# Optimization experiments

Hardware: AMD Instinct MI355X
Metric: run time of the kernel (lower is better)

The kernel has to match this reference:

```python
import jax, jax.numpy as jnp
import numpy as np

DT = 0.1
B_SZ = 8192
T_HIST = 20
LEN_PRED = 30
FEAT = 32
N_LAYERS = 3
# state transition for constant-acceleration model (matches self.F in torch)
F_MAT = np.array([[1.0, DT, DT * DT / 2], [0.0, 1.0, DT], [0.0, 0.0, 1.0]], dtype=np.float32)


def setup_inputs() -> dict:
    key = jax.random.key(0)
    ks = jax.random.split(key, 16)
    # random-walk trajectories as history observations
    hist = jnp.cumsum(jax.random.normal(ks[0], (B_SZ, T_HIST, 2), jnp.float32) * 0.5, axis=1)
    k_lin = 1.0 / np.sqrt(FEAT)
    k_in = 1.0 / np.sqrt(24)

    def u(k, shape, scale):
        return jax.random.uniform(k, shape, jnp.float32, -scale, scale)

    return {
        "hist": hist,
        "max_accel_x": jnp.ones((1,), jnp.float32) * 10.0,
        "max_accel_y": jnp.ones((1,), jnp.float32) * 20.0,
        "velocity_std_x": jnp.ones((1,), jnp.float32) * 10.0,
        "acceleration_std_x": jnp.ones((1,), jnp.float32) * 10.0,
        "R_x_": jnp.array([0.0448], jnp.float32),
        "R_y_": jnp.array([0.001], jnp.float32),
        "G_x": jnp.array([0.0059, 0.2981, 0.0393], jnp.float32),
        "G_y": jnp.array([0.0059, 0.2981, 0.0393], jnp.float32) / 5.0,
        "Win_W": u(ks[1], (FEAT, 24), k_in),
        "Win_b": u(ks[2], (FEAT,), k_in),
        "enc_Wih": u(ks[3], (N_LAYERS, 4 * FEAT, FEAT), k_lin),
        "enc_Whh": u(ks[4], (N_LAYERS, 4 * FEAT, FEAT), k_lin),
        "enc_bih": u(ks[5], (N_LAYERS, 4 * FEAT), k_lin),
        "enc_bhh": u(ks[6], (N_LAYERS, 4 * FEAT), k_lin),
        "dec_Wih": u(ks[7], (N_LAYERS, 4 * FEAT, FEAT), k_lin),
        "dec_Whh": u(ks[8], (N_LAYERS, 4 * FEAT, FEAT), k_lin),
        "dec_bih": u(ks[9], (N_LAYERS, 4 * FEAT), k_lin),
        "dec_bhh": u(ks[10], (N_LAYERS, 4 * FEAT), k_lin),
        "Wout_W": u(ks[11], (4, FEAT), k_lin),
        "Wout_b": u(ks[12], (4,), k_lin),
        "len_pred": LEN_PRED,
    }


def reference(hist, max_accel_x, max_accel_y, velocity_std_x, acceleration_std_x,
              R_x_, R_y_, G_x, G_y, Win_W, Win_b,
              enc_Wih, enc_Whh, enc_bih, enc_bhh,
              dec_Wih, dec_Whh, dec_bih, dec_bhh,
              Wout_W, Wout_b, len_pred):
    B = hist.shape[0]
    F = jnp.asarray(F_MAT)
    R_x = R_x_[0] * R_x_[0]
    R_y = R_y_[0] * R_y_[0]
    Z_x = hist[:, :, 0]
    Z_y = hist[:, :, 1]

    def lstm(x, h, c, Wih, Whh, bih, bhh):
        g = x @ Wih.T + bih + h @ Whh.T + bhh
        i, f, gg, o = jnp.split(g, 4, axis=1)
        c = jax.nn.sigmoid(f) * c + jax.nn.sigmoid(i) * jnp.tanh(gg)
        h = jax.nn.sigmoid(o) * jnp.tanh(c)
        return h, c

    def stack(XP, h, c, Wih, Whh, bih, bhh):
        x = jnp.tanh(XP @ Win_W.T + Win_b)
        hs, cs = [], []
        for j in range(N_LAYERS):
            hj, cj = lstm(x, h[j], c[j], Wih[j], Whh[j], bih[j], bhh[j])
            hs.append(hj)
            cs.append(cj)
            x = cj  # torch code feeds the fresh CELL state to the next layer
        return jnp.stack(hs), jnp.stack(cs)

    def kpred(X, P, Q):
        return X @ F.T, jnp.einsum('ij,bjk,lk->bil', F, P, F) + Q

    def kupdate(X, P, z, R):
        y = z - X[:, 0]                      # innovation (H picks component 0)
        S = P[:, 0, 0] + R                   # innovation covariance (scalar)
        K = P[:, :, 0] / S[:, None]          # Kalman gain (B,3)
        return X + y[:, None] * K, P - K[:, :, None] * P[:, 0:1, :]

    def kinit(z0):
        # torch always calls _kalman_init with is_x=True (default), so both
        # axes use R_x / velocity_std_x / acceleration_std_x
        X = jnp.zeros((B, 3), hist.dtype).at[:, 0].set(z0)
        d = jnp.stack([R_x, velocity_std_x[0] ** 2, acceleration_std_x[0] ** 2])
        P = jnp.zeros((B, 3, 3), hist.dtype).at[:, jnp.arange(3), jnp.arange(3)].set(d)
        return X, P

    Qx_e = jnp.outer(G_x * max_accel_x[0], G_x * max_accel_x[0])
    Qy_e = jnp.outer(G_y * max_accel_y[0], G_y * max_accel_y[0])

    Xx, Px = kinit(Z_x[:, 0])
    Xy, Py = kinit(Z_y[:, 0])
    h = jnp.zeros((N_LAYERS, B, FEAT), hist.dtype)
    c = jnp.zeros_like(h)

    def enc_step(carry, zs):
        Xx, Px, Xy, Py, h, c = carry
        zx, zy = zs
        XP = jnp.concatenate([Xx, Xy, Px.reshape(B, 9), Py.reshape(B, 9)], 1)
        h, c = stack(XP, h, c, enc_Wih, enc_Whh, enc_bih, enc_bhh)
        Xx, Px = kpred(Xx, Px, Qx_e)
        Xy, Py = kpred(Xy, Py, Qy_e)
        Xx, Px = kupdate(Xx, Px, zx, R_x)
        Xy, Py = kupdate(Xy, Py, zy, R_y)
        return (Xx, Px, Xy, Py, h, c), None

    carry, _ = jax.lax.scan(enc_step, (Xx, Px, Xy, Py, h, c),
                            (Z_x[:, 1:].T, Z_y[:, 1:].T))

    oxx = jnp.outer(G_x, G_x)
    oyy = jnp.outer(G_y, G_y)

    def dec_step(carry, _):
        Xx, Px, Xy, Py, h, c = carry
        XP = jnp.concatenate([Xx, Xy, Px.reshape(B, 9), Py.reshape(B, 9)], 1)
        h, c = stack(XP, h, c, dec_Wih, dec_Whh, dec_bih, dec_bhh)
        pred = c[-1] @ Wout_W.T + Wout_b  # (B,4): [u_x, u_y, std_x, std_y]
        Xx = Xx.at[:, 2].set(DT * pred[:, 0])  # X[:,2] = B*u
        Xy = Xy.at[:, 2].set(DT * pred[:, 1])
        Qx = (pred[:, 2] ** 2)[:, None, None] * oxx
        Qy = (pred[:, 3] ** 2)[:, None, None] * oyy
        Xx, Px = kpred(Xx, Px, Qx)
        Xy, Py = kpred(Xy, Py, Qy)
        out = jnp.stack([Xx[:, 0], Xy[:, 0],
                         jnp.sqrt(Px[:, 0, 0]), jnp.sqrt(Py[:, 0, 0]),
                         jnp.zeros(B, hist.dtype)], axis=1)  # (B,5)
        return (Xx, Px, Xy, Py, h, c), out

    carry, ys = jax.lax.scan(dec_step, carry, None, length=len_pred)
    return jnp.transpose(ys, (1, 0, 2))  # (B, len_pred, 5)
```

## Files before the change

### kernel.cpp

```cpp
#include <hip/hip_runtime.h>
#include <math.h>

#define DT   0.1f
#define HDT  0.005f
#define T_HIST 20
#define LEN_PRED 30
#define NLOG2E   (-1.4426950408889634f)
#define TWOLOG2E ( 2.8853900817779268f)

typedef __attribute__((ext_vector_type(8))) short bfrag8;
typedef __attribute__((ext_vector_type(4))) float f32x4;

#define WS_FRAG  0u
#define WS_WIN   98304u
#define WS_WOUT  100352u
#define WS_BIASC 101376u
#define WS_WINC  102912u
#define WS_WOUTB 103040u

static __device__ __forceinline__ unsigned short f2bf(float x) {
    union { float f; unsigned int u; } v; v.f = x;
    unsigned int r = v.u + 0x7fffu + ((v.u >> 16) & 1u);
    return (unsigned short)(r >> 16);
}

static __device__ __forceinline__ unsigned int pack2bf(float lo, float hi) {
    unsigned int ul = __float_as_uint(lo) + 0x8000u;
    unsigned int uh = __float_as_uint(hi) + 0x8000u;
    return __builtin_amdgcn_perm(uh, ul, 0x07060302u);
}

static __device__ __forceinline__ float rcp1(float z) {
    return __builtin_amdgcn_rcpf(1.f + __builtin_amdgcn_exp2f(z));
}
static __device__ __forceinline__ float th_(float z) {
    return fmaf(-2.f, rcp1(z), 1.f);
}

__global__ void prep_kernel(const float* __restrict__ Win_W, const float* __restrict__ Win_b,
                            const float* __restrict__ eWih, const float* __restrict__ eWhh,
                            const float* __restrict__ ebih, const float* __restrict__ ebhh,
                            const float* __restrict__ dWih, const float* __restrict__ dWhh,
                            const float* __restrict__ dbih, const float* __restrict__ dbhh,
                            const float* __restrict__ Wout_W, const float* __restrict__ Wout_b,
                            char* __restrict__ ws)
{
    int i = blockIdx.x * blockDim.x + threadIdx.x;
    if (i < 49152) {
        int fi = i >> 9, w = i & 511;
        int lane = w >> 3, jj = w & 7;
        int c = fi & 1, j = (fi >> 1) & 7, pl = fi >> 4;
        int l = pl % 3, ph = pl / 3;
        int mm = lane & 15, qq = lane >> 4;
        int gate = mm & 3;
        int row = gate * 32 + 8 * (mm >> 2) + j;
        int k = qq * 8 + jj;
        float scale = (gate == 2) ? TWOLOG2E : NLOG2E;
        const float* W = c ? (ph ? dWhh : eWhh) : (ph ? dWih : eWih);
        ((unsigned short*)(ws + WS_FRAG))[i] = f2bf(W[l * 4096 + row * 32 + k] * scale);
    } else if (i < 50176) {
        int i2 = i - 49152;
        int T = i2 >> 9, w = i2 & 511;
        int lane = w >> 3, jj = w & 7;
        int mm = lane & 15, qq = lane >> 4;
        int feat = 8 * (mm >> 2) + 4 * T + (mm & 3);
        int k = qq * 8 + jj;
        float v = (k < 24) ? Win_W[feat * 24 + k] * TWOLOG2E : 0.f;
        ((unsigned short*)(ws + WS_WIN))[i2] = f2bf(v);
    } else if (i < 50688) {
        int i3 = i - 50176;
        int lane = i3 >> 3, jj = i3 & 7;
        int mm = lane & 15, qq = lane >> 4;
        float v = (mm < 4) ? Wout_W[mm * 32 + qq * 8 + jj] : 0.f;
        ((unsigned short*)(ws + WS_WOUT))[i3] = f2bf(v);
    } else if (i < 51072) {
        int b = i - 50688;
        int r = b & 3, qq = (b >> 2) & 3, j = (b >> 4) & 7, pl = b >> 7;
        int l = pl % 3, ph = pl / 3;
        int row = r * 32 + 8 * qq + j;
        float scale = (r == 2) ? TWOLOG2E : NLOG2E;
        const float* bi = ph ? dbih : ebih;
        const float* bh = ph ? dbhh : ebhh;
        ((float*)(ws + WS_BIASC))[b] = (bi[l * 128 + row] + bh[l * 128 + row]) * scale;
    } else if (i < 51104) {
        int b = i - 51072;
        int r = b & 3, qq = (b >> 2) & 3, T = b >> 4;
        ((float*)(ws + WS_WINC))[b] = Win_b[8 * qq + 4 * T + r] * TWOLOG2E;
    } else if (i < 51108) {
        ((float*)(ws + WS_WOUTB))[i - 51104] = Wout_b[i - 51104];
    }
}

__launch_bounds__(64)
__global__ void kalman_lstm_kernel(const float* __restrict__ hist,
                                   const float* __restrict__ max_ax, const float* __restrict__ max_ay,
                                   const float* __restrict__ vstd, const float* __restrict__ astd,
                                   const float* __restrict__ Rx_, const float* __restrict__ Ry_,
                                   const float* __restrict__ Gx, const float* __restrict__ Gy,
                                   const char* __restrict__ ws, float* __restrict__ out)
{
    __shared__ unsigned short xp[16][40];

    const int lane = threadIdx.x;
    const int q = lane >> 4, m = lane & 15, ch = q & 1;
    const int b_elem = blockIdx.x * 16 + m;

    for (int i = lane; i < 640; i += 64) (&xp[0][0])[i] = 0;
    __builtin_amdgcn_wave_barrier();

    bfrag8 fragA[3][8][2];
    f32x4  biasC[3][8];
    const bfrag8* fragp = (const bfrag8*)(ws + WS_FRAG);
    const f32x4*  biasp = (const f32x4*)(ws + WS_BIASC);
    auto load_phase = [&](int ph) {
#pragma unroll
        for (int l = 0; l < 3; ++l)
#pragma unroll
            for (int j = 0; j < 8; ++j) {
#pragma unroll
                for (int c = 0; c < 2; ++c)
                    fragA[l][j][c] = fragp[(((ph * 3 + l) * 8 + j) * 2 + c) * 64 + lane];
                biasC[l][j] = biasp[((ph * 3 + l) * 8 + j) * 4 + q];
            }
    };
    load_phase(0);

    bfrag8 winF0 = ((const bfrag8*)(ws + WS_WIN))[lane];
    bfrag8 winF1 = ((const bfrag8*)(ws + WS_WIN))[64 + lane];
    f32x4  winC0 = ((const f32x4*)(ws + WS_WINC))[q];
    f32x4  winC1 = ((const f32x4*)(ws + WS_WINC))[4 + q];
    bfrag8 woutF = ((const bfrag8*)(ws + WS_WOUT))[lane];
    const float* wbp = (const float*)(ws + WS_WOUTB);
    const float wb0 = wbp[0], wb1 = wbp[1], wb2 = wbp[2], wb3 = wbp[3];

    const float rx = Rx_[0] * Rx_[0], ry = Ry_[0] * Ry_[0];
    const float Rch = ch ? ry : rx;
    float g0, g1, g2, s;
    if (ch == 0) { g0 = Gx[0]; g1 = Gx[1]; g2 = Gx[2]; s = max_ax[0]; }
    else         { g0 = Gy[0]; g1 = Gy[1]; g2 = Gy[2]; s = max_ay[0]; }
    const float ge0 = g0 * s, ge1 = g1 * s, ge2 = g2 * s;
    float X0 = (q < 2) ? hist[b_elem * 40 + ch] : 0.f;
    float X1 = 0.f, X2 = 0.f;
    float P00 = Rch, P01 = 0.f, P02 = 0.f;
    float P11 = vstd[0] * vstd[0], P12 = 0.f, P22 = astd[0] * astd[0];

    union { unsigned int u[4]; bfrag8 v; } zf; zf.u[0] = zf.u[1] = zf.u[2] = zf.u[3] = 0;
    bfrag8 hfrag[3] = { zf.v, zf.v, zf.v };
    float cst[3][8];
#pragma unroll
    for (int l = 0; l < 3; ++l)
#pragma unroll
        for (int j = 0; j < 8; ++j) cst[l][j] = 0.f;
    bfrag8 xfrag = zf.v;

    auto kpred = [&](float Q00, float Q01, float Q02, float Q11, float Q12, float Q22) {
        X0 = X0 + DT * X1 + HDT * X2;
        X1 = X1 + DT * X2;
        float M00 = P00 + DT * P01 + HDT * P02;
        float M01 = P01 + DT * P11 + HDT * P12;
        float M02 = P02 + DT * P12 + HDT * P22;
        float M11 = P11 + DT * P12;
        float M12 = P12 + DT * P22;
        float M22 = P22;
        P00 = M00 + DT * M01 + HDT * M02 + Q00;
        P01 = M01 + DT * M02 + Q01;
        P02 = M02 + Q02;
        P11 = M11 + DT * M12 + Q11;
        P12 = M12 + Q12;
        P22 = M22 + Q22;
    };
    auto kupdate = [&](float z) {
        float y = z - X0;
        float Sinv = 1.0f / (P00 + Rch);
        float K0 = P00 * Sinv, K1 = P01 * Sinv, K2 = P02 * Sinv;
        X0 += y * K0; X1 += y * K1; X2 += y * K2;
        float p00 = P00, p01 = P01, p02 = P02;
        P00 = p00 - K0 * p00;
        P01 = p01 - K0 * p01;
        P02 = p02 - K0 * p02;
        P11 = P11 - K1 * p01;
        P12 = P12 - K1 * p02;
        P22 = P22 - K2 * p02;
    };

    auto stack = [&]() {
        if (q < 2) {
            unsigned short* row = &xp[m][0];
            int o = ch * 3;
            row[o + 0] = f2bf(X0); row[o + 1] = f2bf(X1); row[o + 2] = f2bf(X2);
            int pb = 6 + ch * 9;
            row[pb + 0] = f2bf(P00); row[pb + 1] = f2bf(P01); row[pb + 2] = f2bf(P02);
            row[pb + 3] = f2bf(P01); row[pb + 4] = f2bf(P11); row[pb + 5] = f2bf(P12);
            row[pb + 6] = f2bf(P02); row[pb + 7] = f2bf(P12); row[pb + 8] = f2bf(P22);
        }
        __builtin_amdgcn_wave_barrier();
        bfrag8 bxp = *(const bfrag8*)&xp[m][q * 8];
        __builtin_amdgcn_wave_barrier();
        f32x4 t0 = __builtin_amdgcn_mfma_f32_16x16x32_bf16(winF0, bxp, winC0, 0, 0, 0);
        f32x4 t1 = __builtin_amdgcn_mfma_f32_16x16x32_bf16(winF1, bxp, winC1, 0, 0, 0);
        union { unsigned int u[4]; bfrag8 v; } xu;
        xu.u[0] = pack2bf(th_(t0[0]), th_(t0[1]));
        xu.u[1] = pack2bf(th_(t0[2]), th_(t0[3]));
        xu.u[2] = pack2bf(th_(t1[0]), th_(t1[1]));
        xu.u[3] = pack2bf(th_(t1[2]), th_(t1[3]));
        xfrag = xu.v;
#pragma unroll
        for (int l = 0; l < 3; ++l) {
            f32x4 acc[8];
#pragma unroll
            for (int j = 0; j < 8; ++j) {
                f32x4 hh = __builtin_amdgcn_mfma_f32_16x16x32_bf16(fragA[l][j][1], hfrag[l], biasC[l][j], 0, 0, 0);
                acc[j]   = __builtin_amdgcn_mfma_f32_16x16x32_bf16(fragA[l][j][0], xfrag, hh, 0, 0, 0);
            }
            union { unsigned int u[4]; bfrag8 v; } xu2, hu2;
#pragma unroll
            for (int jp = 0; jp < 4; ++jp) {
                float cn[2], hn[2];
#pragma unroll
                for (int e = 0; e < 2; ++e) {
                    int j = jp * 2 + e;
                    float iv = rcp1(acc[j][0]);
                    float fv = rcp1(acc[j][1]);
                    float gv = th_(acc[j][2]);
                    float ov = rcp1(acc[j][3]);
                    float cv = fmaf(fv, cst[l][j], iv * gv);
                    cst[l][j] = cv;
                    float tc = th_(cv * TWOLOG2E);
                    cn[e] = cv; hn[e] = ov * tc;
                }
                xu2.u[jp] = pack2bf(cn[0], cn[1]);
                hu2.u[jp] = pack2bf(hn[0], hn[1]);
            }
            xfrag = xu2.v;
            hfrag[l] = hu2.v;
        }
    };

    const f32x4 zero4 = {0.f, 0.f, 0.f, 0.f};

    float znext = (q < 2) ? hist[b_elem * 40 + 2 + ch] : 0.f;
#pragma unroll 1
    for (int t = 0; t < T_HIST - 1; ++t) {
        stack();
        float z = znext;
        if (t < 18) znext = (q < 2) ? hist[b_elem * 40 + (t + 2) * 2 + ch] : 0.f;
        kpred(ge0 * ge0, ge0 * ge1, ge0 * ge2, ge1 * ge1, ge1 * ge2, ge2 * ge2);
        kupdate(z);
    }

    load_phase(1);

#pragma unroll 1
    for (int t = 0; t < LEN_PRED; ++t) {
        stack();
        f32x4 ap = __builtin_amdgcn_mfma_f32_16x16x32_bf16(woutF, xfrag, zero4, 0, 0, 0);
        float s0 = __shfl(ap[0] + wb0, m);
        float s1 = __shfl(ap[1] + wb1, m);
        float s2 = __shfl(ap[2] + wb2, m);
        float s3 = __shfl(ap[3] + wb3, m);
        float pe = ch ? s1 : s0;
        float qe = ch ? s3 : s2;
        X2 = DT * pe;
        float qs = qe * qe;
        kpred(qs * g0 * g0, qs * g0 * g1, qs * g0 * g2, qs * g1 * g1, qs * g1 * g2, qs * g2 * g2);
        if (q < 2) {
            float* o = out + (size_t)b_elem * (LEN_PRED * 5) + t * 5;
            if (ch == 0) { o[0] = X0; o[2] = sqrtf(P00); }
            else         { o[1] = X0; o[3] = sqrtf(P00); o[4] = 0.f; }
        }
    }
}

extern "C" void kernel_launch(void* const* d_in, const int* in_sizes, int n_in,
                              void* d_out, int out_size, void* d_ws, size_t ws_size,
                              hipStream_t stream)
{
    const float* hist  = (const float*)d_in[0];
    const float* maxax = (const float*)d_in[1];
    const float* maxay = (const float*)d_in[2];
    const float* vstd  = (const float*)d_in[3];
    const float* astd  = (const float*)d_in[4];
    const float* Rx    = (const float*)d_in[5];
    const float* Ry    = (const float*)d_in[6];
    const float* Gx    = (const float*)d_in[7];
    const float* Gy    = (const float*)d_in[8];
    const float* WinW  = (const float*)d_in[9];
    const float* Winb  = (const float*)d_in[10];
    const float* eWih  = (const float*)d_in[11];
    const float* eWhh  = (const float*)d_in[12];
    const float* ebih  = (const float*)d_in[13];
    const float* ebhh  = (const float*)d_in[14];
    const float* dWih  = (const float*)d_in[15];
    const float* dWhh  = (const float*)d_in[16];
    const float* dbih  = (const float*)d_in[17];
    const float* dbhh  = (const float*)d_in[18];
    const float* WoutW = (const float*)d_in[19];
    const float* Woutb = (const float*)d_in[20];
    char* ws = (char*)d_ws;
    float* out = (float*)d_out;

    prep_kernel<<<200, 256, 0, stream>>>(WinW, Winb, eWih, eWhh, ebih, ebhh,
                                         dWih, dWhh, dbih, dbhh, WoutW, Woutb, ws);
    kalman_lstm_kernel<<<512, 64, 0, stream>>>(hist, maxax, maxay, vstd, astd,
                                               Rx, Ry, Gx, Gy, ws, out);
}
```

Baseline: 217.1 us.

## Halve batch per wave and split LSTM cell nonlinearities across half-lanes

Each wave now handles 8 batch elements instead of 16, and the grid doubles to 1024 waves. Lanes with m>=8 take over the elementwise gate math for feature columns 4-7 via shfl_xor, halving the serial transcendental work per lane. Results are exchanged back with shuffles to rebuild the bf16 fragments. The trade is twice the MFMA work overall (half the MFMA columns are wasted) and extra shuffles, in exchange for shorter per-step latency and more waves to fill the GPU.

```diff
diff --git a/kernel.cpp b/kernel.cpp
--- a/kernel.cpp
+++ b/kernel.cpp
@@ -103,7 +103,8 @@
 
     const int lane = threadIdx.x;
     const int q = lane >> 4, m = lane & 15, ch = q & 1;
-    const int b_elem = blockIdx.x * 16 + m;
+    const bool act = (m < 8);
+    const int b_elem = blockIdx.x * 8 + (m & 7);
 
     for (int i = lane; i < 640; i += 64) (&xp[0][0])[i] = 0;
     __builtin_amdgcn_wave_barrier();
@@ -139,19 +140,19 @@
     if (ch == 0) { g0 = Gx[0]; g1 = Gx[1]; g2 = Gx[2]; s = max_ax[0]; }
     else         { g0 = Gy[0]; g1 = Gy[1]; g2 = Gy[2]; s = max_ay[0]; }
     const float ge0 = g0 * s, ge1 = g1 * s, ge2 = g2 * s;
-    float X0 = (q < 2) ? hist[b_elem * 40 + ch] : 0.f;
+    float X0 = (q < 2 && act) ? hist[b_elem * 40 + ch] : 0.f;
     float X1 = 0.f, X2 = 0.f;
     float P00 = Rch, P01 = 0.f, P02 = 0.f;
     float P11 = vstd[0] * vstd[0], P12 = 0.f, P22 = astd[0] * astd[0];
 
     union { unsigned int u[4]; bfrag8 v; } zf; zf.u[0] = zf.u[1] = zf.u[2] = zf.u[3] = 0;
     bfrag8 hfrag[3] = { zf.v, zf.v, zf.v };
-    float cst[3][8];
+    bfrag8 xfrag = zf.v;
+    float cst[3][4];
 #pragma unroll
     for (int l = 0; l < 3; ++l)
 #pragma unroll
-        for (int j = 0; j < 8; ++j) cst[l][j] = 0.f;
-    bfrag8 xfrag = zf.v;
+        for (int k = 0; k < 4; ++k) cst[l][k] = 0.f;
 
     auto kpred = [&](float Q00, float Q01, float Q02, float Q11, float Q12, float Q22) {
         X0 = X0 + DT * X1 + HDT * X2;
@@ -184,7 +185,7 @@
     };
 
     auto stack = [&]() {
-        if (q < 2) {
+        if (q < 2 && act) {
             unsigned short* row = &xp[m][0];
             int o = ch * 3;
             row[o + 0] = f2bf(X0); row[o + 1] = f2bf(X1); row[o + 2] = f2bf(X2);
@@ -212,38 +213,44 @@
                 f32x4 hh = __builtin_amdgcn_mfma_f32_16x16x32_bf16(fragA[l][j][1], hfrag[l], biasC[l][j], 0, 0, 0);
                 acc[j]   = __builtin_amdgcn_mfma_f32_16x16x32_bf16(fragA[l][j][0], xfrag, hh, 0, 0, 0);
             }
-            union { unsigned int u[4]; bfrag8 v; } xu2, hu2;
-#pragma unroll
-            for (int jp = 0; jp < 4; ++jp) {
-                float cn[2], hn[2];
-#pragma unroll
-                for (int e = 0; e < 2; ++e) {
-                    int j = jp * 2 + e;
-                    float iv = rcp1(acc[j][0]);
-                    float fv = rcp1(acc[j][1]);
-                    float gv = th_(acc[j][2]);
-                    float ov = rcp1(acc[j][3]);
-                    float cv = fmaf(fv, cst[l][j], iv * gv);
-                    cst[l][j] = cv;
-                    float tc = th_(cv * TWOLOG2E);
-                    cn[e] = cv; hn[e] = ov * tc;
-                }
-                xu2.u[jp] = pack2bf(cn[0], cn[1]);
-                hu2.u[jp] = pack2bf(hn[0], hn[1]);
+            float cn[4], hn[4];
+#pragma unroll
+            for (int k = 0; k < 4; ++k) {
+                float s0 = __shfl_xor(acc[k + 4][0], 8);
+                float s1 = __shfl_xor(acc[k + 4][1], 8);
+                float s2 = __shfl_xor(acc[k + 4][2], 8);
+                float s3 = __shfl_xor(acc[k + 4][3], 8);
+                float gi = act ? acc[k][0] : s0;
+                float gf = act ? acc[k][1] : s1;
+                float gg = act ? acc[k][2] : s2;
+                float go = act ? acc[k][3] : s3;
+                float iv = rcp1(gi);
+                float fv = rcp1(gf);
+                float gv = th_(gg);
+                float ov = rcp1(go);
+                float cv = fmaf(fv, cst[l][k], iv * gv);
+                cst[l][k] = cv;
+                cn[k] = cv;
+                hn[k] = ov * th_(cv * TWOLOG2E);
             }
-            xfrag = xu2.v;
-            hfrag[l] = hu2.v;
+            union { unsigned int u[4]; bfrag8 v; } xv, hv;
+            xv.u[0] = pack2bf(cn[0], cn[1]); xv.u[1] = pack2bf(cn[2], cn[3]);
+            hv.u[0] = pack2bf(hn[0], hn[1]); hv.u[1] = pack2bf(hn[2], hn[3]);
+            xv.u[2] = __shfl_xor(xv.u[0], 8); xv.u[3] = __shfl_xor(xv.u[1], 8);
+            hv.u[2] = __shfl_xor(hv.u[0], 8); hv.u[3] = __shfl_xor(hv.u[1], 8);
+            xfrag = xv.v;
+            hfrag[l] = hv.v;
         }
     };
 
     const f32x4 zero4 = {0.f, 0.f, 0.f, 0.f};
 
-    float znext = (q < 2) ? hist[b_elem * 40 + 2 + ch] : 0.f;
+    float znext = (q < 2 && act) ? hist[b_elem * 40 + 2 + ch] : 0.f;
 #pragma unroll 1
     for (int t = 0; t < T_HIST - 1; ++t) {
         stack();
         float z = znext;
-        if (t < 18) znext = (q < 2) ? hist[b_elem * 40 + (t + 2) * 2 + ch] : 0.f;
+        if (t < 18) znext = (q < 2 && act) ? hist[b_elem * 40 + (t + 2) * 2 + ch] : 0.f;
         kpred(ge0 * ge0, ge0 * ge1, ge0 * ge2, ge1 * ge1, ge1 * ge2, ge2 * ge2);
         kupdate(z);
     }
@@ -263,7 +270,7 @@
         X2 = DT * pe;
         float qs = qe * qe;
         kpred(qs * g0 * g0, qs * g0 * g1, qs * g0 * g2, qs * g1 * g1, qs * g1 * g2, qs * g2 * g2);
-        if (q < 2) {
+        if (q < 2 && act) {
             float* o = out + (size_t)b_elem * (LEN_PRED * 5) + t * 5;
             if (ch == 0) { o[0] = X0; o[2] = sqrtf(P00); }
             else         { o[1] = X0; o[3] = sqrtf(P00); o[4] = 0.f; }
@@ -301,6 +308,6 @@
 
     prep_kernel<<<200, 256, 0, stream>>>(WinW, Winb, eWih, eWhh, ebih, ebhh,
                                          dWih, dWhh, dbih, dbhh, WoutW, Woutb, ws);
-    kalman_lstm_kernel<<<512, 64, 0, stream>>>(hist, maxax, maxay, vstd, astd,
-                                               Rx, Ry, Gx, Gy, ws, out);
-}
+    kalman_lstm_kernel<<<1024, 64, 0, stream>>>(hist, maxax, maxay, vstd, astd,
+                                                Rx, Ry, Gx, Gy, ws, out);
+}
```

After: 212.1 us. -2.3%, faster.
